# Performance work log

Measured on AMD Instinct MI355X. Metric: run time of the kernel, lower is better.

The kernel has to match this reference:

```python
import jax, jax.numpy as jnp
import numpy as np

N_USER = 100000
N_ITEM = 100000
E = 1000000
D_IN = 64
D_OUT = 64


def setup_inputs() -> dict:
    key = jax.random.key(0)
    ks = jax.random.split(key, 10)
    scale = 1.0 / np.sqrt(D_IN)
    return {
        "feat_user": jax.random.normal(ks[0], (N_USER, D_IN), jnp.float32),
        "feat_item": jax.random.normal(ks[1], (N_ITEM, D_IN), jnp.float32),
        "src_clicks": jax.random.randint(ks[2], (E,), 0, N_USER),        # user ids
        "dst_clicks": jax.random.randint(ks[3], (E,), 0, N_ITEM),        # item ids
        "src_clicked_by": jax.random.randint(ks[4], (E,), 0, N_ITEM),    # item ids
        "dst_clicked_by": jax.random.randint(ks[5], (E,), 0, N_USER),    # user ids
        "W_clicks": jax.random.normal(ks[6], (D_OUT, D_IN), jnp.float32) * scale,
        "b_clicks": jax.random.normal(ks[7], (D_OUT,), jnp.float32) * scale,
        "W_clicked_by": jax.random.normal(ks[8], (D_OUT, D_IN), jnp.float32) * scale,
        "b_clicked_by": jax.random.normal(ks[9], (D_OUT,), jnp.float32) * scale,
    }


def _relation_mean(feat_src, W, b, src, dst, n_dst):
    # per-relation Linear on src features (nn.Linear: x @ W.T + b)
    Wh = feat_src @ W.T + b                                  # [N_src, D_OUT]
    # copy_u + mean: gather messages along edges, segment-mean at dst
    msum = jax.ops.segment_sum(Wh[src], dst, num_segments=n_dst)   # [n_dst, D_OUT]
    deg = jax.ops.segment_sum(jnp.ones(src.shape[0], jnp.float32), dst,
                              num_segments=n_dst)                   # [n_dst]
    return msum / jnp.maximum(deg, 1.0)[:, None]             # zero-degree dsts -> 0


def reference(feat_user, feat_item, src_clicks, dst_clicks,
              src_clicked_by, dst_clicked_by,
              W_clicks, b_clicks, W_clicked_by, b_clicked_by):
    # relation (user, clicks, item): messages land on item nodes
    h_item = _relation_mean(feat_user, W_clicks, b_clicks,
                            src_clicks, dst_clicks, N_ITEM)
    # relation (item, clicked_by, user): messages land on user nodes
    h_user = _relation_mean(feat_item, W_clicked_by, b_clicked_by,
                            src_clicked_by, dst_clicked_by, N_USER)
    # cross-relation 'sum' reducer: each ntype receives from exactly one relation here
    return (h_user, h_item)
```

## Files before the change

kernel.cpp:

```cpp
#include <hip/hip_runtime.h>
#include <hip/hip_fp16.h>

#define D 64
#define BSH 7
#define BK 128
#define NBK 1024
#define CAP 2048
#define CHUNK 4096
#define EPT (CHUNK / 256)
#define TILE 128

static __device__ __forceinline__ unsigned short f2h(float x) {
    __half h = __float2half(x);
    return *(unsigned short*)&h;
}

__global__ __launch_bounds__(256) void phase1(
    const float* __restrict__ feat_u, const float* __restrict__ feat_i,
    const float* __restrict__ W_c, const float* __restrict__ b_c,
    const float* __restrict__ W_cb, const float* __restrict__ b_cb,
    unsigned short* __restrict__ Whb_u, unsigned short* __restrict__ Whb_i,
    const int* __restrict__ srcA, const int* __restrict__ dstA,
    const int* __restrict__ srcB, const int* __restrict__ dstB,
    int* __restrict__ bcur,
    unsigned int* __restrict__ ebufA, unsigned int* __restrict__ ebufB,
    int n_user, int n_item, int n_edges, int ntile, int eb) {
    __shared__ union {
        struct { float FT[D * TILE]; float WT[D * D]; } lin;
        struct { int hist[NBK], cur[NBK]; } fil;
    } sh;
    int t = threadIdx.x;
    int blk = blockIdx.x;

    if (blk < 2 * ntile) {
        int rel = (blk >= ntile);
        int tile = rel ? blk - ntile : blk;
        const float* feat = rel ? feat_i : feat_u;
        const float* W    = rel ? W_cb   : W_c;
        const float* bia  = rel ? b_cb   : b_c;
        unsigned short* out = rel ? Whb_i : Whb_u;
        int n = rel ? n_item : n_user;
        int row0 = tile * TILE;
        if (row0 >= n) return;
        int kq = t & 15;
        int rr = t >> 4;
        int k4 = kq * 4;
        #pragma unroll
        for (int g = 0; g < 8; ++g) {
            int r = rr + g * 16;
            int grow = row0 + r; if (grow > n - 1) grow = n - 1;
            float4 f = *(const float4*)(feat + (size_t)grow * D + k4);
            int sw = ((((r >> 2) ^ kq) & 31) << 2) + (r & 3);
            sh.lin.FT[(k4 + 0) * TILE + sw] = f.x;
            sh.lin.FT[(k4 + 1) * TILE + sw] = f.y;
            sh.lin.FT[(k4 + 2) * TILE + sw] = f.z;
            sh.lin.FT[(k4 + 3) * TILE + sw] = f.w;
        }
        #pragma unroll
        for (int g = 0; g < 4; ++g) {
            int c = rr + g * 16;
            float4 w = *(const float4*)(W + c * D + k4);
            int swc = ((((c >> 2) ^ kq) & 15) << 2) + (c & 3);
            sh.lin.WT[(k4 + 0) * D + swc] = w.x;
            sh.lin.WT[(k4 + 1) * D + swc] = w.y;
            sh.lin.WT[(k4 + 2) * D + swc] = w.z;
            sh.lin.WT[(k4 + 3) * D + swc] = w.w;
        }
        __syncthreads();
        int cb = t & 15;
        int rb = t >> 4;
        int c0 = cb * 4;
        int r0 = rb * 8;
        float4 bv = *(const float4*)(bia + c0);
        float acc[8][4];
        #pragma unroll
        for (int ri = 0; ri < 8; ++ri) {
            acc[ri][0] = bv.x; acc[ri][1] = bv.y; acc[ri][2] = bv.z; acc[ri][3] = bv.w;
        }
        #pragma unroll 4
        for (int k = 0; k < D; ++k) {
            int kq2 = k >> 2;
            float4 w  = *(const float4*)(sh.lin.WT + k * D    + (((cb ^ kq2) & 15) << 2));
            float4 fA = *(const float4*)(sh.lin.FT + k * TILE + ((((rb * 2)     ^ kq2) & 31) << 2));
            float4 fB = *(const float4*)(sh.lin.FT + k * TILE + ((((rb * 2 + 1) ^ kq2) & 31) << 2));
            float fr[8] = {fA.x, fA.y, fA.z, fA.w, fB.x, fB.y, fB.z, fB.w};
            #pragma unroll
            for (int ri = 0; ri < 8; ++ri) {
                acc[ri][0] = fmaf(fr[ri], w.x, acc[ri][0]);
                acc[ri][1] = fmaf(fr[ri], w.y, acc[ri][1]);
                acc[ri][2] = fmaf(fr[ri], w.z, acc[ri][2]);
                acc[ri][3] = fmaf(fr[ri], w.w, acc[ri][3]);
            }
        }
        #pragma unroll
        for (int ri = 0; ri < 8; ++ri) {
            int row = row0 + r0 + ri;
            if (row < n) {
                ushort4 o;
                o.x = f2h(acc[ri][0]); o.y = f2h(acc[ri][1]);
                o.z = f2h(acc[ri][2]); o.w = f2h(acc[ri][3]);
                *(ushort4*)(out + (size_t)row * D + c0) = o;
            }
        }
    } else {
        int fb = blk - 2 * ntile;
        int rel = (fb >= eb);
        int chunk = rel ? fb - eb : fb;
        const int* src = rel ? srcB : srcA;
        const int* dst = rel ? dstB : dstA;
        int* bu = bcur + rel * NBK;
        unsigned int* ebuf = rel ? ebufB : ebufA;
        int base = chunk * CHUNK;
        int m = n_edges - base; if (m > CHUNK) m = CHUNK;
        unsigned int packed[EPT];
        int bk[EPT];
        if (m == CHUNK) {
            const int4* s4p = (const int4*)(src + base);
            const int4* d4p = (const int4*)(dst + base);
            int4 sv[EPT / 4], dv[EPT / 4];
            #pragma unroll
            for (int q = 0; q < EPT / 4; ++q) {
                sv[q] = s4p[t * (EPT / 4) + q];
                dv[q] = d4p[t * (EPT / 4) + q];
            }
            for (int i = t; i < NBK; i += 256) sh.fil.hist[i] = 0;
            __syncthreads();
            #pragma unroll
            for (int q = 0; q < EPT / 4; ++q) {
                int s4a[4] = {sv[q].x, sv[q].y, sv[q].z, sv[q].w};
                int d4a[4] = {dv[q].x, dv[q].y, dv[q].z, dv[q].w};
                #pragma unroll
                for (int jj = 0; jj < 4; ++jj) {
                    int j = q * 4 + jj;
                    bk[j] = ((unsigned)d4a[jj]) >> BSH;
                    packed[j] = (unsigned int)s4a[jj] | (((unsigned int)d4a[jj] & (BK - 1)) << 24);
                    atomicAdd(&sh.fil.hist[bk[j]], 1);
                }
            }
        } else {
            for (int i = t; i < NBK; i += 256) sh.fil.hist[i] = 0;
            __syncthreads();
            #pragma unroll
            for (int j = 0; j < EPT; ++j) {
                int e = base + t * EPT + j;
                if (e < n_edges) {
                    int d = dst[e];
                    int s = src[e];
                    bk[j] = ((unsigned)d) >> BSH;
                    packed[j] = (unsigned int)s | (((unsigned int)d & (BK - 1)) << 24);
                    atomicAdd(&sh.fil.hist[bk[j]], 1);
                } else bk[j] = -1;
            }
        }
        __syncthreads();
        for (int b2 = t; b2 < NBK; b2 += 256) {
            int c = sh.fil.hist[b2];
            if (c) sh.fil.cur[b2] = b2 * CAP + atomicAdd(&bu[b2], c);
        }
        __syncthreads();
        #pragma unroll
        for (int j = 0; j < EPT; ++j) {
            if (bk[j] >= 0) {
                int pos = atomicAdd(&sh.fil.cur[bk[j]], 1);
                if ((unsigned)(pos - bk[j] * CAP) < CAP)
                    ebuf[pos] = packed[j];
            }
        }
    }
}

__global__ __launch_bounds__(256) void bucket_gather(
    const unsigned short* __restrict__ Whb_u, const unsigned short* __restrict__ Whb_i,
    const unsigned int* __restrict__ ebufA, const unsigned int* __restrict__ ebufB,
    const int* __restrict__ bcur,
    float* __restrict__ h_user, float* __restrict__ h_item,
    int n_user, int n_item) {
    int rel = blockIdx.y;
    const unsigned short* Wh = rel ? Whb_u : Whb_i;
    const unsigned int* ebuf = rel ? ebufB : ebufA;
    float* out = rel ? h_item : h_user;
    int n = rel ? n_item : n_user;
    int b = blockIdx.x;
    int cnt = bcur[rel * NBK + b]; if (cnt > CAP) cnt = CAP;
    size_t base = (size_t)b * CAP;
    __shared__ unsigned int ssrc[CAP];
    __shared__ int hist[BK], ofs[BK], cur[BK];
    __shared__ int w0tot;
    int t = threadIdx.x;
    if (t < BK) hist[t] = 0;
    __syncthreads();
    unsigned int pk[CAP / 256];
    #pragma unroll
    for (int j = 0; j < CAP / 256; ++j) {
        int i = t + j * 256;
        if (i < cnt) {
            pk[j] = ebuf[base + i];
            atomicAdd(&hist[pk[j] >> 24], 1);
        }
    }
    __syncthreads();
    {
        int lane = t & 63;
        int v = (t < BK) ? hist[t] : 0;
        int inc = v;
        #pragma unroll
        for (int o = 1; o < 64; o <<= 1) {
            int x = __shfl_up(inc, o, 64);
            if (lane >= o) inc += x;
        }
        if (t == 63) w0tot = inc;
        __syncthreads();
        if (t >= 64 && t < BK) inc += w0tot;
        if (t < BK) { int ex = inc - v; ofs[t] = ex; cur[t] = ex; }
    }
    __syncthreads();
    #pragma unroll
    for (int j = 0; j < CAP / 256; ++j) {
        int i = t + j * 256;
        if (i < cnt) {
            int nd = pk[j] >> 24;
            int p = atomicAdd(&cur[nd], 1);
            ssrc[p] = pk[j] & 0xFFFFFFu;
        }
    }
    __syncthreads();
    int lane = t & 63;
    int w = t >> 6;
    int half = lane >> 5;
    int lp = lane & 31;
    int node0 = b * BK;
    for (int nd = w; nd < BK; nd += 4) {
        int node = node0 + nd;
        if (node >= n) break;
        int st = ofs[nd];
        int dg = hist[nd];
        int en = st + dg;
        __half2 hs[8];
        #pragma unroll
        for (int q = 0; q < 8; ++q) hs[q] = __float2half2_rn(0.f);
        for (int j = st; j < en; j += 16) {
            unsigned int v[8];
            #pragma unroll
            for (int q = 0; q < 8; ++q) {
                int e = j + 2 * q + half;
                v[q] = 0u;
                if (e < en) v[q] = ((const unsigned int*)(Wh + (size_t)ssrc[e] * D))[lp];
            }
            #pragma unroll
            for (int q = 0; q < 8; ++q)
                hs[q] = __hadd2(hs[q], *(const __half2*)&v[q]);
        }
        __half2 s0 = __hadd2(__hadd2(hs[0], hs[1]), __hadd2(hs[2], hs[3]));
        __half2 s1 = __hadd2(__hadd2(hs[4], hs[5]), __hadd2(hs[6], hs[7]));
        __half2 s  = __hadd2(s0, s1);
        float lo = __low2float(s);
        float hi = __high2float(s);
        lo += __shfl_xor(lo, 32, 64);
        hi += __shfl_xor(hi, 32, 64);
        if (half == 0) {
            float inv = 1.f / fmaxf((float)dg, 1.f);
            float2 o; o.x = lo * inv; o.y = hi * inv;
            *(float2*)(out + (size_t)node * D + 2 * lp) = o;
        }
    }
}

extern "C" void kernel_launch(void* const* d_in, const int* in_sizes, int n_in,
                              void* d_out, int out_size, void* d_ws, size_t ws_size,
                              hipStream_t stream) {
    const float* feat_user      = (const float*)d_in[0];
    const float* feat_item      = (const float*)d_in[1];
    const int*   src_clicks     = (const int*)d_in[2];
    const int*   dst_clicks     = (const int*)d_in[3];
    const int*   src_clicked_by = (const int*)d_in[4];
    const int*   dst_clicked_by = (const int*)d_in[5];
    const float* W_clicks       = (const float*)d_in[6];
    const float* b_clicks       = (const float*)d_in[7];
    const float* W_clicked_by   = (const float*)d_in[8];
    const float* b_clicked_by   = (const float*)d_in[9];

    const int n_user  = in_sizes[0] / D;
    const int n_item  = in_sizes[1] / D;
    const int n_edges = in_sizes[2];

    float* out = (float*)d_out;
    float* h_user = out;
    float* h_item = out + (size_t)n_user * D;

    unsigned short* Whb_user = (unsigned short*)d_ws;
    unsigned short* Whb_item = Whb_user + (size_t)n_user * D;
    int* ip        = (int*)(Whb_item + (size_t)n_item * D);
    unsigned int* ebuf_user = (unsigned int*)ip;  ip += NBK * CAP;
    unsigned int* ebuf_item = (unsigned int*)ip;  ip += NBK * CAP;
    int* bcur = ip;

    hipMemsetAsync(bcur, 0, 2 * NBK * sizeof(int), stream);

    int ntile = (max(n_user, n_item) + TILE - 1) / TILE;
    int eb = (n_edges + CHUNK - 1) / CHUNK;
    phase1<<<2 * ntile + 2 * eb, 256, 0, stream>>>(
        feat_user, feat_item, W_clicks, b_clicks, W_clicked_by, b_clicked_by,
        Whb_user, Whb_item,
        src_clicked_by, dst_clicked_by, src_clicks, dst_clicks,
        bcur, ebuf_user, ebuf_item,
        n_user, n_item, n_edges, ntile, eb);

    int nbkt = (max(n_user, n_item) + BK - 1) / BK;
    bucket_gather<<<dim3(nbkt, 2), 256, 0, stream>>>(
        Whb_user, Whb_item, ebuf_user, ebuf_item, bcur,
        h_user, h_item, n_user, n_item);
}
```

Before: 201.6 us.

## Fuse memset, linear/bucketing and gather into one cooperative persistent kernel

Replaces the memset plus two kernel launches with a single cooperative kernel that zeroes the bucket counters, runs the linear and edge-bucketing tasks in a grid-stride loop, grid-syncs, then runs the bucket-gather tasks. It aims to remove launch overhead and the gaps between the three stages. In exchange the grid is capped by occupancy, the shared-memory union grows, and grid.sync barriers are added. The grid size is computed once and cached in a static variable.

```diff
diff --git a/kernel.cpp b/kernel.cpp
--- a/kernel.cpp
+++ b/kernel.cpp
@@ -1,5 +1,8 @@
 #include <hip/hip_runtime.h>
 #include <hip/hip_fp16.h>
+#include <hip/hip_cooperative_groups.h>
+
+namespace cg = cooperative_groups;
 
 #define D 64
 #define BSH 7
@@ -15,7 +18,7 @@
     return *(unsigned short*)&h;
 }
 
-__global__ __launch_bounds__(256) void phase1(
+__global__ __launch_bounds__(256) void fused(
     const float* __restrict__ feat_u, const float* __restrict__ feat_i,
     const float* __restrict__ W_c, const float* __restrict__ b_c,
     const float* __restrict__ W_cb, const float* __restrict__ b_cb,
@@ -24,244 +27,252 @@
     const int* __restrict__ srcB, const int* __restrict__ dstB,
     int* __restrict__ bcur,
     unsigned int* __restrict__ ebufA, unsigned int* __restrict__ ebufB,
-    int n_user, int n_item, int n_edges, int ntile, int eb) {
+    float* __restrict__ h_user, float* __restrict__ h_item,
+    int n_user, int n_item, int n_edges, int ntile, int eb, int nbkt) {
     __shared__ union {
         struct { float FT[D * TILE]; float WT[D * D]; } lin;
         struct { int hist[NBK], cur[NBK]; } fil;
+        struct { unsigned int ssrc[CAP]; int hist[BK], ofs[BK], cur[BK]; int w0tot; } gat;
     } sh;
     int t = threadIdx.x;
-    int blk = blockIdx.x;
-
-    if (blk < 2 * ntile) {
-        int rel = (blk >= ntile);
-        int tile = rel ? blk - ntile : blk;
-        const float* feat = rel ? feat_i : feat_u;
-        const float* W    = rel ? W_cb   : W_c;
-        const float* bia  = rel ? b_cb   : b_c;
-        unsigned short* out = rel ? Whb_i : Whb_u;
-        int n = rel ? n_item : n_user;
-        int row0 = tile * TILE;
-        if (row0 >= n) return;
-        int kq = t & 15;
-        int rr = t >> 4;
-        int k4 = kq * 4;
-        #pragma unroll
-        for (int g = 0; g < 8; ++g) {
-            int r = rr + g * 16;
-            int grow = row0 + r; if (grow > n - 1) grow = n - 1;
-            float4 f = *(const float4*)(feat + (size_t)grow * D + k4);
-            int sw = ((((r >> 2) ^ kq) & 31) << 2) + (r & 3);
-            sh.lin.FT[(k4 + 0) * TILE + sw] = f.x;
-            sh.lin.FT[(k4 + 1) * TILE + sw] = f.y;
-            sh.lin.FT[(k4 + 2) * TILE + sw] = f.z;
-            sh.lin.FT[(k4 + 3) * TILE + sw] = f.w;
-        }
-        #pragma unroll
-        for (int g = 0; g < 4; ++g) {
-            int c = rr + g * 16;
-            float4 w = *(const float4*)(W + c * D + k4);
-            int swc = ((((c >> 2) ^ kq) & 15) << 2) + (c & 3);
-            sh.lin.WT[(k4 + 0) * D + swc] = w.x;
-            sh.lin.WT[(k4 + 1) * D + swc] = w.y;
-            sh.lin.WT[(k4 + 2) * D + swc] = w.z;
-            sh.lin.WT[(k4 + 3) * D + swc] = w.w;
+    cg::grid_group grid = cg::this_grid();
+
+    for (int i = blockIdx.x * 256 + t; i < 2 * NBK; i += gridDim.x * 256) bcur[i] = 0;
+    grid.sync();
+
+    int ntaskA = 2 * ntile + 2 * eb;
+    for (int task = blockIdx.x; task < ntaskA; task += gridDim.x) {
+        if (task < 2 * ntile) {
+            int rel = (task >= ntile);
+            int tile = rel ? task - ntile : task;
+            const float* feat = rel ? feat_i : feat_u;
+            const float* W    = rel ? W_cb   : W_c;
+            const float* bia  = rel ? b_cb   : b_c;
+            unsigned short* out = rel ? Whb_i : Whb_u;
+            int n = rel ? n_item : n_user;
+            int row0 = tile * TILE;
+            if (row0 < n) {
+                int kq = t & 15;
+                int rr = t >> 4;
+                int k4 = kq * 4;
+                #pragma unroll
+                for (int g = 0; g < 8; ++g) {
+                    int r = rr + g * 16;
+                    int grow = row0 + r; if (grow > n - 1) grow = n - 1;
+                    float4 f = *(const float4*)(feat + (size_t)grow * D + k4);
+                    int sw = ((((r >> 2) ^ kq) & 31) << 2) + (r & 3);
+                    sh.lin.FT[(k4 + 0) * TILE + sw] = f.x;
+                    sh.lin.FT[(k4 + 1) * TILE + sw] = f.y;
+                    sh.lin.FT[(k4 + 2) * TILE + sw] = f.z;
+                    sh.lin.FT[(k4 + 3) * TILE + sw] = f.w;
+                }
+                #pragma unroll
+                for (int g = 0; g < 4; ++g) {
+                    int c = rr + g * 16;
+                    float4 w = *(const float4*)(W + c * D + k4);
+                    int swc = ((((c >> 2) ^ kq) & 15) << 2) + (c & 3);
+                    sh.lin.WT[(k4 + 0) * D + swc] = w.x;
+                    sh.lin.WT[(k4 + 1) * D + swc] = w.y;
+                    sh.lin.WT[(k4 + 2) * D + swc] = w.z;
+                    sh.lin.WT[(k4 + 3) * D + swc] = w.w;
+                }
+                __syncthreads();
+                int cb = t & 15;
+                int rb = t >> 4;
+                int c0 = cb * 4;
+                int r0 = rb * 8;
+                float4 bv = *(const float4*)(bia + c0);
+                float acc[8][4];
+                #pragma unroll
+                for (int ri = 0; ri < 8; ++ri) {
+                    acc[ri][0] = bv.x; acc[ri][1] = bv.y; acc[ri][2] = bv.z; acc[ri][3] = bv.w;
+                }
+                #pragma unroll 4
+                for (int k = 0; k < D; ++k) {
+                    int kq2 = k >> 2;
+                    float4 w  = *(const float4*)(sh.lin.WT + k * D    + (((cb ^ kq2) & 15) << 2));
+                    float4 fA = *(const float4*)(sh.lin.FT + k * TILE + ((((rb * 2)     ^ kq2) & 31) << 2));
+                    float4 fB = *(const float4*)(sh.lin.FT + k * TILE + ((((rb * 2 + 1) ^ kq2) & 31) << 2));
+                    float fr[8] = {fA.x, fA.y, fA.z, fA.w, fB.x, fB.y, fB.z, fB.w};
+                    #pragma unroll
+                    for (int ri = 0; ri < 8; ++ri) {
+                        acc[ri][0] = fmaf(fr[ri], w.x, acc[ri][0]);
+                        acc[ri][1] = fmaf(fr[ri], w.y, acc[ri][1]);
+                        acc[ri][2] = fmaf(fr[ri], w.z, acc[ri][2]);
+                        acc[ri][3] = fmaf(fr[ri], w.w, acc[ri][3]);
+                    }
+                }
+                #pragma unroll
+                for (int ri = 0; ri < 8; ++ri) {
+                    int row = row0 + r0 + ri;
+                    if (row < n) {
+                        ushort4 o;
+                        o.x = f2h(acc[ri][0]); o.y = f2h(acc[ri][1]);
+                        o.z = f2h(acc[ri][2]); o.w = f2h(acc[ri][3]);
+                        *(ushort4*)(out + (size_t)row * D + c0) = o;
+                    }
+                }
+            }
+        } else {
+            int fb = task - 2 * ntile;
+            int rel = (fb >= eb);
+            int chunk = rel ? fb - eb : fb;
+            const int* src = rel ? srcB : srcA;
+            const int* dst = rel ? dstB : dstA;
+            int* bu = bcur + rel * NBK;
+            unsigned int* ebuf = rel ? ebufB : ebufA;
+            int base = chunk * CHUNK;
+            int m = n_edges - base; if (m > CHUNK) m = CHUNK;
+            unsigned int packed[EPT];
+            int bk[EPT];
+            if (m == CHUNK) {
+                const int4* s4p = (const int4*)(src + base);
+                const int4* d4p = (const int4*)(dst + base);
+                int4 sv[EPT / 4], dv[EPT / 4];
+                #pragma unroll
+                for (int q = 0; q < EPT / 4; ++q) {
+                    sv[q] = s4p[t * (EPT / 4) + q];
+                    dv[q] = d4p[t * (EPT / 4) + q];
+                }
+                for (int i = t; i < NBK; i += 256) sh.fil.hist[i] = 0;
+                __syncthreads();
+                #pragma unroll
+                for (int q = 0; q < EPT / 4; ++q) {
+                    int s4a[4] = {sv[q].x, sv[q].y, sv[q].z, sv[q].w};
+                    int d4a[4] = {dv[q].x, dv[q].y, dv[q].z, dv[q].w};
+                    #pragma unroll
+                    for (int jj = 0; jj < 4; ++jj) {
+                        int j = q * 4 + jj;
+                        bk[j] = ((unsigned)d4a[jj]) >> BSH;
+                        packed[j] = (unsigned int)s4a[jj] | (((unsigned int)d4a[jj] & (BK - 1)) << 24);
+                        atomicAdd(&sh.fil.hist[bk[j]], 1);
+                    }
+                }
+            } else {
+                for (int i = t; i < NBK; i += 256) sh.fil.hist[i] = 0;
+                __syncthreads();
+                #pragma unroll
+                for (int j = 0; j < EPT; ++j) {
+                    int e = base + t * EPT + j;
+                    if (e < n_edges) {
+                        int d = dst[e];
+                        int s = src[e];
+                        bk[j] = ((unsigned)d) >> BSH;
+                        packed[j] = (unsigned int)s | (((unsigned int)d & (BK - 1)) << 24);
+                        atomicAdd(&sh.fil.hist[bk[j]], 1);
+                    } else bk[j] = -1;
+                }
+            }
+            __syncthreads();
+            for (int b2 = t; b2 < NBK; b2 += 256) {
+                int c = sh.fil.hist[b2];
+                if (c) sh.fil.cur[b2] = b2 * CAP + atomicAdd(&bu[b2], c);
+            }
+            __syncthreads();
+            #pragma unroll
+            for (int j = 0; j < EPT; ++j) {
+                if (bk[j] >= 0) {
+                    int pos = atomicAdd(&sh.fil.cur[bk[j]], 1);
+                    if ((unsigned)(pos - bk[j] * CAP) < CAP)
+                        ebuf[pos] = packed[j];
+                }
+            }
         }
         __syncthreads();
-        int cb = t & 15;
-        int rb = t >> 4;
-        int c0 = cb * 4;
-        int r0 = rb * 8;
-        float4 bv = *(const float4*)(bia + c0);
-        float acc[8][4];
-        #pragma unroll
-        for (int ri = 0; ri < 8; ++ri) {
-            acc[ri][0] = bv.x; acc[ri][1] = bv.y; acc[ri][2] = bv.z; acc[ri][3] = bv.w;
-        }
-        #pragma unroll 4
-        for (int k = 0; k < D; ++k) {
-            int kq2 = k >> 2;
-            float4 w  = *(const float4*)(sh.lin.WT + k * D    + (((cb ^ kq2) & 15) << 2));
-            float4 fA = *(const float4*)(sh.lin.FT + k * TILE + ((((rb * 2)     ^ kq2) & 31) << 2));
-            float4 fB = *(const float4*)(sh.lin.FT + k * TILE + ((((rb * 2 + 1) ^ kq2) & 31) << 2));
-            float fr[8] = {fA.x, fA.y, fA.z, fA.w, fB.x, fB.y, fB.z, fB.w};
+    }
+
+    __threadfence();
+    grid.sync();
+
+    int ntaskC = 2 * nbkt;
+    for (int task = blockIdx.x; task < ntaskC; task += gridDim.x) {
+        int rel = (task >= nbkt);
+        int b = rel ? task - nbkt : task;
+        const unsigned short* Wh = rel ? Whb_u : Whb_i;
+        const unsigned int* ebuf = rel ? ebufB : ebufA;
+        float* out = rel ? h_item : h_user;
+        int n = rel ? n_item : n_user;
+        int node0 = b * BK;
+        if (node0 < n) {
+            int cnt = bcur[rel * NBK + b]; if (cnt > CAP) cnt = CAP;
+            size_t base = (size_t)b * CAP;
+            if (t < BK) sh.gat.hist[t] = 0;
+            __syncthreads();
+            unsigned int pk[CAP / 256];
             #pragma unroll
-            for (int ri = 0; ri < 8; ++ri) {
-                acc[ri][0] = fmaf(fr[ri], w.x, acc[ri][0]);
-                acc[ri][1] = fmaf(fr[ri], w.y, acc[ri][1]);
-                acc[ri][2] = fmaf(fr[ri], w.z, acc[ri][2]);
-                acc[ri][3] = fmaf(fr[ri], w.w, acc[ri][3]);
-            }
-        }
-        #pragma unroll
-        for (int ri = 0; ri < 8; ++ri) {
-            int row = row0 + r0 + ri;
-            if (row < n) {
-                ushort4 o;
-                o.x = f2h(acc[ri][0]); o.y = f2h(acc[ri][1]);
-                o.z = f2h(acc[ri][2]); o.w = f2h(acc[ri][3]);
-                *(ushort4*)(out + (size_t)row * D + c0) = o;
-            }
-        }
-    } else {
-        int fb = blk - 2 * ntile;
-        int rel = (fb >= eb);
-        int chunk = rel ? fb - eb : fb;
-        const int* src = rel ? srcB : srcA;
-        const int* dst = rel ? dstB : dstA;
-        int* bu = bcur + rel * NBK;
-        unsigned int* ebuf = rel ? ebufB : ebufA;
-        int base = chunk * CHUNK;
-        int m = n_edges - base; if (m > CHUNK) m = CHUNK;
-        unsigned int packed[EPT];
-        int bk[EPT];
-        if (m == CHUNK) {
-            const int4* s4p = (const int4*)(src + base);
-            const int4* d4p = (const int4*)(dst + base);
-            int4 sv[EPT / 4], dv[EPT / 4];
+            for (int j = 0; j < CAP / 256; ++j) {
+                int i = t + j * 256;
+                if (i < cnt) {
+                    pk[j] = ebuf[base + i];
+                    atomicAdd(&sh.gat.hist[pk[j] >> 24], 1);
+                }
+            }
+            __syncthreads();
+            {
+                int lane = t & 63;
+                int v = (t < BK) ? sh.gat.hist[t] : 0;
+                int inc = v;
+                #pragma unroll
+                for (int o = 1; o < 64; o <<= 1) {
+                    int x = __shfl_up(inc, o, 64);
+                    if (lane >= o) inc += x;
+                }
+                if (t == 63) sh.gat.w0tot = inc;
+                __syncthreads();
+                if (t >= 64 && t < BK) inc += sh.gat.w0tot;
+                if (t < BK) { int ex = inc - v; sh.gat.ofs[t] = ex; sh.gat.cur[t] = ex; }
+            }
+            __syncthreads();
             #pragma unroll
-            for (int q = 0; q < EPT / 4; ++q) {
-                sv[q] = s4p[t * (EPT / 4) + q];
-                dv[q] = d4p[t * (EPT / 4) + q];
-            }
-            for (int i = t; i < NBK; i += 256) sh.fil.hist[i] = 0;
-            __syncthreads();
-            #pragma unroll
-            for (int q = 0; q < EPT / 4; ++q) {
-                int s4a[4] = {sv[q].x, sv[q].y, sv[q].z, sv[q].w};
-                int d4a[4] = {dv[q].x, dv[q].y, dv[q].z, dv[q].w};
-                #pragma unroll
-                for (int jj = 0; jj < 4; ++jj) {
-                    int j = q * 4 + jj;
-                    bk[j] = ((unsigned)d4a[jj]) >> BSH;
-                    packed[j] = (unsigned int)s4a[jj] | (((unsigned int)d4a[jj] & (BK - 1)) << 24);
-                    atomicAdd(&sh.fil.hist[bk[j]], 1);
-                }
-            }
-        } else {
-            for (int i = t; i < NBK; i += 256) sh.fil.hist[i] = 0;
-            __syncthreads();
-            #pragma unroll
-            for (int j = 0; j < EPT; ++j) {
-                int e = base + t * EPT + j;
-                if (e < n_edges) {
-                    int d = dst[e];
-                    int s = src[e];
-                    bk[j] = ((unsigned)d) >> BSH;
-                    packed[j] = (unsigned int)s | (((unsigned int)d & (BK - 1)) << 24);
-                    atomicAdd(&sh.fil.hist[bk[j]], 1);
-                } else bk[j] = -1;
+            for (int j = 0; j < CAP / 256; ++j) {
+                int i = t + j * 256;
+                if (i < cnt) {
+                    int nd = pk[j] >> 24;
+                    int p = atomicAdd(&sh.gat.cur[nd], 1);
+                    sh.gat.ssrc[p] = pk[j] & 0xFFFFFFu;
+                }
+            }
+            __syncthreads();
+            int lane = t & 63;
+            int w = t >> 6;
+            int half = lane >> 5;
+            int lp = lane & 31;
+            for (int nd = w; nd < BK; nd += 4) {
+                int node = node0 + nd;
+                if (node >= n) break;
+                int st = sh.gat.ofs[nd];
+                int dg = sh.gat.hist[nd];
+                int en = st + dg;
+                __half2 hs[8];
+                #pragma unroll
+                for (int q = 0; q < 8; ++q) hs[q] = __float2half2_rn(0.f);
+                for (int j = st; j < en; j += 16) {
+                    unsigned int v[8];
+                    #pragma unroll
+                    for (int q = 0; q < 8; ++q) {
+                        int e = j + 2 * q + half;
+                        v[q] = 0u;
+                        if (e < en) v[q] = ((const unsigned int*)(Wh + (size_t)sh.gat.ssrc[e] * D))[lp];
+                    }
+                    #pragma unroll
+                    for (int q = 0; q < 8; ++q)
+                        hs[q] = __hadd2(hs[q], *(const __half2*)&v[q]);
+                }
+                __half2 s0 = __hadd2(__hadd2(hs[0], hs[1]), __hadd2(hs[2], hs[3]));
+                __half2 s1 = __hadd2(__hadd2(hs[4], hs[5]), __hadd2(hs[6], hs[7]));
+                __half2 s  = __hadd2(s0, s1);
+                float lo = __low2float(s);
+                float hi = __high2float(s);
+                lo += __shfl_xor(lo, 32, 64);
+                hi += __shfl_xor(hi, 32, 64);
+                if (half == 0) {
+                    float inv = 1.f / fmaxf((float)dg, 1.f);
+                    float2 o; o.x = lo * inv; o.y = hi * inv;
+                    *(float2*)(out + (size_t)node * D + 2 * lp) = o;
+                }
             }
         }
         __syncthreads();
-        for (int b2 = t; b2 < NBK; b2 += 256) {
-            int c = sh.fil.hist[b2];
-            if (c) sh.fil.cur[b2] = b2 * CAP + atomicAdd(&bu[b2], c);
-        }
-        __syncthreads();
-        #pragma unroll
-        for (int j = 0; j < EPT; ++j) {
-            if (bk[j] >= 0) {
-                int pos = atomicAdd(&sh.fil.cur[bk[j]], 1);
-                if ((unsigned)(pos - bk[j] * CAP) < CAP)
-                    ebuf[pos] = packed[j];
-            }
-        }
-    }
-}
-
-__global__ __launch_bounds__(256) void bucket_gather(
-    const unsigned short* __restrict__ Whb_u, const unsigned short* __restrict__ Whb_i,
-    const unsigned int* __restrict__ ebufA, const unsigned int* __restrict__ ebufB,
-    const int* __restrict__ bcur,
-    float* __restrict__ h_user, float* __restrict__ h_item,
-    int n_user, int n_item) {
-    int rel = blockIdx.y;
-    const unsigned short* Wh = rel ? Whb_u : Whb_i;
-    const unsigned int* ebuf = rel ? ebufB : ebufA;
-    float* out = rel ? h_item : h_user;
-    int n = rel ? n_item : n_user;
-    int b = blockIdx.x;
-    int cnt = bcur[rel * NBK + b]; if (cnt > CAP) cnt = CAP;
-    size_t base = (size_t)b * CAP;
-    __shared__ unsigned int ssrc[CAP];
-    __shared__ int hist[BK], ofs[BK], cur[BK];
-    __shared__ int w0tot;
-    int t = threadIdx.x;
-    if (t < BK) hist[t] = 0;
-    __syncthreads();
-    unsigned int pk[CAP / 256];
-    #pragma unroll
-    for (int j = 0; j < CAP / 256; ++j) {
-        int i = t + j * 256;
-        if (i < cnt) {
-            pk[j] = ebuf[base + i];
-            atomicAdd(&hist[pk[j] >> 24], 1);
-        }
-    }
-    __syncthreads();
-    {
-        int lane = t & 63;
-        int v = (t < BK) ? hist[t] : 0;
-        int inc = v;
-        #pragma unroll
-        for (int o = 1; o < 64; o <<= 1) {
-            int x = __shfl_up(inc, o, 64);
-            if (lane >= o) inc += x;
-        }
-        if (t == 63) w0tot = inc;
-        __syncthreads();
-        if (t >= 64 && t < BK) inc += w0tot;
-        if (t < BK) { int ex = inc - v; ofs[t] = ex; cur[t] = ex; }
-    }
-    __syncthreads();
-    #pragma unroll
-    for (int j = 0; j < CAP / 256; ++j) {
-        int i = t + j * 256;
-        if (i < cnt) {
-            int nd = pk[j] >> 24;
-            int p = atomicAdd(&cur[nd], 1);
-            ssrc[p] = pk[j] & 0xFFFFFFu;
-        }
-    }
-    __syncthreads();
-    int lane = t & 63;
-    int w = t >> 6;
-    int half = lane >> 5;
-    int lp = lane & 31;
-    int node0 = b * BK;
-    for (int nd = w; nd < BK; nd += 4) {
-        int node = node0 + nd;
-        if (node >= n) break;
-        int st = ofs[nd];
-        int dg = hist[nd];
-        int en = st + dg;
-        __half2 hs[8];
-        #pragma unroll
-        for (int q = 0; q < 8; ++q) hs[q] = __float2half2_rn(0.f);
-        for (int j = st; j < en; j += 16) {
-            unsigned int v[8];
-            #pragma unroll
-            for (int q = 0; q < 8; ++q) {
-                int e = j + 2 * q + half;
-                v[q] = 0u;
-                if (e < en) v[q] = ((const unsigned int*)(Wh + (size_t)ssrc[e] * D))[lp];
-            }
-            #pragma unroll
-            for (int q = 0; q < 8; ++q)
-                hs[q] = __hadd2(hs[q], *(const __half2*)&v[q]);
-        }
-        __half2 s0 = __hadd2(__hadd2(hs[0], hs[1]), __hadd2(hs[2], hs[3]));
-        __half2 s1 = __hadd2(__hadd2(hs[4], hs[5]), __hadd2(hs[6], hs[7]));
-        __half2 s  = __hadd2(s0, s1);
-        float lo = __low2float(s);
-        float hi = __high2float(s);
-        lo += __shfl_xor(lo, 32, 64);
-        hi += __shfl_xor(hi, 32, 64);
-        if (half == 0) {
-            float inv = 1.f / fmaxf((float)dg, 1.f);
-            float2 o; o.x = lo * inv; o.y = hi * inv;
-            *(float2*)(out + (size_t)node * D + 2 * lp) = o;
-        }
     }
 }
 
@@ -294,19 +305,27 @@
     unsigned int* ebuf_item = (unsigned int*)ip;  ip += NBK * CAP;
     int* bcur = ip;
 
-    hipMemsetAsync(bcur, 0, 2 * NBK * sizeof(int), stream);
-
     int ntile = (max(n_user, n_item) + TILE - 1) / TILE;
     int eb = (n_edges + CHUNK - 1) / CHUNK;
-    phase1<<<2 * ntile + 2 * eb, 256, 0, stream>>>(
-        feat_user, feat_item, W_clicks, b_clicks, W_clicked_by, b_clicked_by,
-        Whb_user, Whb_item,
-        src_clicked_by, dst_clicked_by, src_clicks, dst_clicks,
-        bcur, ebuf_user, ebuf_item,
-        n_user, n_item, n_edges, ntile, eb);
-
     int nbkt = (max(n_user, n_item) + BK - 1) / BK;
-    bucket_gather<<<dim3(nbkt, 2), 256, 0, stream>>>(
-        Whb_user, Whb_item, ebuf_user, ebuf_item, bcur,
-        h_user, h_item, n_user, n_item);
+
+    static int grid = 0;
+    if (grid == 0) {
+        int maxb = 0;
+        if (hipOccupancyMaxActiveBlocksPerMultiprocessor(&maxb, fused, 256, 0) != hipSuccess
+            || maxb < 1) maxb = 2;
+        grid = maxb * 256;
+        if (grid > 1536) grid = 1536;
+    }
+
+    void* args[] = {
+        (void*)&feat_user, (void*)&feat_item,
+        (void*)&W_clicks, (void*)&b_clicks, (void*)&W_clicked_by, (void*)&b_clicked_by,
+        (void*)&Whb_user, (void*)&Whb_item,
+        (void*)&src_clicked_by, (void*)&dst_clicked_by, (void*)&src_clicks, (void*)&dst_clicks,
+        (void*)&bcur, (void*)&ebuf_user, (void*)&ebuf_item,
+        (void*)&h_user, (void*)&h_item,
+        (void*)&n_user, (void*)&n_item, (void*)&n_edges, (void*)&ntile, (void*)&eb, (void*)&nbkt
+    };
+    hipLaunchCooperativeKernel((const void*)fused, dim3(grid), dim3(256), args, 0, stream);
 }
```

Measured after the change: 475.9 us. 136% more time.
